# Kernel tuning notes

Measured on AMD Instinct MI355X. Metric: run time of the kernel, lower is better.

Reference implementation:

```python
import jax, jax.numpy as jnp
import numpy as np


def setup_inputs() -> dict:
    key = jax.random.key(0)
    k1, k2, k3 = jax.random.split(key, 3)
    x = jax.random.normal(k1, (16, 64, 256, 256), dtype=jnp.float32)
    # Conv2d(2, 1, kernel_size=7, padding=3): weight [out=1, in=2, 7, 7], bias [1]
    fan_in = 2 * 7 * 7
    bound = 1.0 / np.sqrt(fan_in)
    conv_w = jax.random.uniform(k2, (1, 2, 7, 7), jnp.float32, -bound, bound)
    conv_b = jax.random.uniform(k3, (1,), jnp.float32, -bound, bound)
    return {"x": x, "conv_w": conv_w, "conv_b": conv_b}


def reference(x, conv_w, conv_b):
    # x: [B, C, H, W]
    avg_out = jnp.mean(x, axis=1, keepdims=True)          # [B,1,H,W]
    max_out = jnp.max(x, axis=1, keepdims=True)           # [B,1,H,W]
    att = jnp.concatenate([avg_out, max_out], axis=1)     # [B,2,H,W]
    att = jax.lax.conv_general_dilated(
        att, conv_w,
        window_strides=(1, 1),
        padding=((3, 3), (3, 3)),
        dimension_numbers=("NCHW", "OIHW", "NCHW"),
    ) + conv_b.reshape(1, 1, 1, 1)                         # [B,1,H,W]
    att = jax.nn.sigmoid(att)
    return x * att
```

## Files before the change

kernel.cpp:

```cpp
#include <hip/hip_runtime.h>
#include <math.h>

#define BB   16
#define CC   64
#define HH_  256
#define WW_  256
#define HW   (HH_ * WW_)
#define CHW  (CC * HW)
#define BH   8
#define HALO 3
#define PR   (BH + 2*HALO)
#define NBANDS (HH_ / BH)
#define NBLK (BB * NBANDS)
#define NT_  512

typedef float vfloat4 __attribute__((ext_vector_type(4)));

__global__ __launch_bounds__(NT_) void fused_kernel(const float* __restrict__ x,
                                                    const float* __restrict__ cw,
                                                    const float* __restrict__ cb,
                                                    float* __restrict__ out) {
    __shared__ float sw[99];
    __shared__ float ap[PR][WW_];
    __shared__ float mp[PR][WW_];

    const int tid = threadIdx.x;
    if (tid < 99) sw[tid] = (tid < 98) ? cw[tid] : cb[0];

    const int bid  = blockIdx.x;
    const int b    = bid >> 5;
    const int band = bid & (NBANDS - 1);
    const int R0   = band * BH;

    const float4* xb4 = (const float4*)x + (size_t)b * (CHW / 4);

    for (int j = tid; j < PR * 64; j += NT_) {
        const int i   = j >> 6;
        const int q   = j & 63;
        const int row = R0 - HALO + i;
        float4 a = {0.f, 0.f, 0.f, 0.f};
        float4 m = {0.f, 0.f, 0.f, 0.f};
        if (row >= 0 && row < HH_) {
            const float4* p = xb4 + row * 64 + q;
            float4 s  = {0.f, 0.f, 0.f, 0.f};
            float4 mm = {-INFINITY, -INFINITY, -INFINITY, -INFINITY};
            #pragma unroll 8
            for (int c = 0; c < CC; ++c) {
                float4 v = p[c * (HW / 4)];
                s.x += v.x; s.y += v.y; s.z += v.z; s.w += v.w;
                mm.x = fmaxf(mm.x, v.x); mm.y = fmaxf(mm.y, v.y);
                mm.z = fmaxf(mm.z, v.z); mm.w = fmaxf(mm.w, v.w);
            }
            const float inv = 1.0f / 64.0f;
            a.x = s.x * inv; a.y = s.y * inv; a.z = s.z * inv; a.w = s.w * inv;
            m = mm;
        }
        *(float4*)&ap[i][q * 4] = a;
        *(float4*)&mp[i][q * 4] = m;
    }
    __syncthreads();

    const float bias = sw[98];

    {
        const int rl  = tid >> 6;
        const int q   = tid & 63;
        const int row = R0 + rl;

        float acc0 = bias, acc1 = bias, acc2 = bias, acc3 = bias;
        #pragma unroll
        for (int dy = -3; dy <= 3; ++dy) {
            const int li = rl + HALO + dy;
            const float4* a4 = (const float4*)&ap[li][0];
            const float4* m4 = (const float4*)&mp[li][0];
            const float4 z = {0.f, 0.f, 0.f, 0.f};
            float4 aL = (q > 0)  ? a4[q - 1] : z;
            float4 aC = a4[q];
            float4 aR = (q < 63) ? a4[q + 1] : z;
            float4 mL = (q > 0)  ? m4[q - 1] : z;
            float4 mC = m4[q];
            float4 mR = (q < 63) ? m4[q + 1] : z;
            float av[12] = {aL.x,aL.y,aL.z,aL.w, aC.x,aC.y,aC.z,aC.w, aR.x,aR.y,aR.z,aR.w};
            float mv[12] = {mL.x,mL.y,mL.z,mL.w, mC.x,mC.y,mC.z,mC.w, mR.x,mR.y,mR.z,mR.w};
            const float* wr = sw + (dy + 3) * 7;
            #pragma unroll
            for (int kx = 0; kx < 7; ++kx) {
                float wa = wr[kx];
                float wm = wr[49 + kx];
                int t = 1 + kx;
                acc0 = fmaf(av[t + 0], wa, acc0);  acc0 = fmaf(mv[t + 0], wm, acc0);
                acc1 = fmaf(av[t + 1], wa, acc1);  acc1 = fmaf(mv[t + 1], wm, acc1);
                acc2 = fmaf(av[t + 2], wa, acc2);  acc2 = fmaf(mv[t + 2], wm, acc2);
                acc3 = fmaf(av[t + 3], wa, acc3);  acc3 = fmaf(mv[t + 3], wm, acc3);
            }
        }

        const float att0 = 1.f / (1.f + __expf(-acc0));
        const float att1 = 1.f / (1.f + __expf(-acc1));
        const float att2 = 1.f / (1.f + __expf(-acc2));
        const float att3 = 1.f / (1.f + __expf(-acc3));

        const vfloat4* xr = (const vfloat4*)x  + (size_t)b * (CHW / 4) + row * 64 + q;
        vfloat4*       ow = (vfloat4*)out      + (size_t)b * (CHW / 4) + row * 64 + q;
        #pragma unroll 4
        for (int c = 0; c < CC; ++c) {
            vfloat4 v = __builtin_nontemporal_load(xr + c * (HW / 4));
            vfloat4 r;
            r.x = v.x * att0; r.y = v.y * att1; r.z = v.z * att2; r.w = v.w * att3;
            __builtin_nontemporal_store(r, ow + c * (HW / 4));
        }
    }
}

extern "C" void kernel_launch(void* const* d_in, const int* in_sizes, int n_in,
                              void* d_out, int out_size, void* d_ws, size_t ws_size,
                              hipStream_t stream) {
    const float* x  = (const float*)d_in[0];
    const float* cw = (const float*)d_in[1];
    const float* cb = (const float*)d_in[2];
    float* out = (float*)d_out;

    fused_kernel<<<dim3(NBLK), dim3(NT_), 0, stream>>>(x, cw, cb, out);
}
```

Measured before the change: 499.8 us.

## Split fused kernel into pool-conv kernel and grid-stride reverse-order scale kernel

Splits the single fused kernel into two. The first computes channel pooling, the 7x7 conv and the sigmoid, using smaller bands (4 rows, 256 threads, twice as many blocks), and writes the attention map to workspace. The second is a flat elementwise scale kernel that walks the tensor in reverse order, so the most recently read part of x is more likely to still be in cache. This raises parallelism in both phases but adds a kernel launch, a round trip of the attention map through memory, and more halo recomputation from the smaller bands.

```diff
diff --git a/kernel.cpp b/kernel.cpp
--- a/kernel.cpp
+++ b/kernel.cpp
@@ -7,19 +7,26 @@
 #define WW_  256
 #define HW   (HH_ * WW_)
 #define CHW  (CC * HW)
-#define BH   8
+#define NPIX (BB * HW)
+
+#define BH   4
 #define HALO 3
 #define PR   (BH + 2*HALO)
 #define NBANDS (HH_ / BH)
 #define NBLK (BB * NBANDS)
-#define NT_  512
+
+#define T4      (NPIX * CC / 4)
+#define K2_BLK  2048
+#define K2_THR  256
+#define K2_STEP (K2_BLK * K2_THR)
+#define K2_IT   (T4 / K2_STEP)
 
 typedef float vfloat4 __attribute__((ext_vector_type(4)));
 
-__global__ __launch_bounds__(NT_) void fused_kernel(const float* __restrict__ x,
-                                                    const float* __restrict__ cw,
-                                                    const float* __restrict__ cb,
-                                                    float* __restrict__ out) {
+__global__ __launch_bounds__(256) void pool_conv_kernel(const float* __restrict__ x,
+                                                        const float* __restrict__ cw,
+                                                        const float* __restrict__ cb,
+                                                        float* __restrict__ att) {
     __shared__ float sw[99];
     __shared__ float ap[PR][WW_];
     __shared__ float mp[PR][WW_];
@@ -28,13 +35,13 @@
     if (tid < 99) sw[tid] = (tid < 98) ? cw[tid] : cb[0];
 
     const int bid  = blockIdx.x;
-    const int b    = bid >> 5;
+    const int b    = bid >> 6;
     const int band = bid & (NBANDS - 1);
     const int R0   = band * BH;
 
     const float4* xb4 = (const float4*)x + (size_t)b * (CHW / 4);
 
-    for (int j = tid; j < PR * 64; j += NT_) {
+    for (int j = tid; j < PR * 64; j += 256) {
         const int i   = j >> 6;
         const int q   = j & 63;
         const int row = R0 - HALO + i;
@@ -44,7 +51,7 @@
             const float4* p = xb4 + row * 64 + q;
             float4 s  = {0.f, 0.f, 0.f, 0.f};
             float4 mm = {-INFINITY, -INFINITY, -INFINITY, -INFINITY};
-            #pragma unroll 8
+            #pragma unroll 16
             for (int c = 0; c < CC; ++c) {
                 float4 v = p[c * (HW / 4)];
                 s.x += v.x; s.y += v.y; s.z += v.z; s.w += v.w;
@@ -61,54 +68,64 @@
     __syncthreads();
 
     const float bias = sw[98];
+    const int rl  = tid >> 6;
+    const int q   = tid & 63;
+    const int row = R0 + rl;
 
-    {
-        const int rl  = tid >> 6;
-        const int q   = tid & 63;
-        const int row = R0 + rl;
+    float acc0 = bias, acc1 = bias, acc2 = bias, acc3 = bias;
+    #pragma unroll
+    for (int dy = -3; dy <= 3; ++dy) {
+        const int li = rl + HALO + dy;
+        const float4* a4 = (const float4*)&ap[li][0];
+        const float4* m4 = (const float4*)&mp[li][0];
+        const float4 z = {0.f, 0.f, 0.f, 0.f};
+        float4 aL = (q > 0)  ? a4[q - 1] : z;
+        float4 aC = a4[q];
+        float4 aR = (q < 63) ? a4[q + 1] : z;
+        float4 mL = (q > 0)  ? m4[q - 1] : z;
+        float4 mC = m4[q];
+        float4 mR = (q < 63) ? m4[q + 1] : z;
+        float av[12] = {aL.x,aL.y,aL.z,aL.w, aC.x,aC.y,aC.z,aC.w, aR.x,aR.y,aR.z,aR.w};
+        float mv[12] = {mL.x,mL.y,mL.z,mL.w, mC.x,mC.y,mC.z,mC.w, mR.x,mR.y,mR.z,mR.w};
+        const float* wr = sw + (dy + 3) * 7;
+        #pragma unroll
+        for (int kx = 0; kx < 7; ++kx) {
+            float wa = wr[kx];
+            float wm = wr[49 + kx];
+            int t = 1 + kx;
+            acc0 = fmaf(av[t + 0], wa, acc0);  acc0 = fmaf(mv[t + 0], wm, acc0);
+            acc1 = fmaf(av[t + 1], wa, acc1);  acc1 = fmaf(mv[t + 1], wm, acc1);
+            acc2 = fmaf(av[t + 2], wa, acc2);  acc2 = fmaf(mv[t + 2], wm, acc2);
+            acc3 = fmaf(av[t + 3], wa, acc3);  acc3 = fmaf(mv[t + 3], wm, acc3);
+        }
+    }
 
-        float acc0 = bias, acc1 = bias, acc2 = bias, acc3 = bias;
-        #pragma unroll
-        for (int dy = -3; dy <= 3; ++dy) {
-            const int li = rl + HALO + dy;
-            const float4* a4 = (const float4*)&ap[li][0];
-            const float4* m4 = (const float4*)&mp[li][0];
-            const float4 z = {0.f, 0.f, 0.f, 0.f};
-            float4 aL = (q > 0)  ? a4[q - 1] : z;
-            float4 aC = a4[q];
-            float4 aR = (q < 63) ? a4[q + 1] : z;
-            float4 mL = (q > 0)  ? m4[q - 1] : z;
-            float4 mC = m4[q];
-            float4 mR = (q < 63) ? m4[q + 1] : z;
-            float av[12] = {aL.x,aL.y,aL.z,aL.w, aC.x,aC.y,aC.z,aC.w, aR.x,aR.y,aR.z,aR.w};
-            float mv[12] = {mL.x,mL.y,mL.z,mL.w, mC.x,mC.y,mC.z,mC.w, mR.x,mR.y,mR.z,mR.w};
-            const float* wr = sw + (dy + 3) * 7;
-            #pragma unroll
-            for (int kx = 0; kx < 7; ++kx) {
-                float wa = wr[kx];
-                float wm = wr[49 + kx];
-                int t = 1 + kx;
-                acc0 = fmaf(av[t + 0], wa, acc0);  acc0 = fmaf(mv[t + 0], wm, acc0);
-                acc1 = fmaf(av[t + 1], wa, acc1);  acc1 = fmaf(mv[t + 1], wm, acc1);
-                acc2 = fmaf(av[t + 2], wa, acc2);  acc2 = fmaf(mv[t + 2], wm, acc2);
-                acc3 = fmaf(av[t + 3], wa, acc3);  acc3 = fmaf(mv[t + 3], wm, acc3);
-            }
-        }
+    float4 attq;
+    attq.x = 1.f / (1.f + __expf(-acc0));
+    attq.y = 1.f / (1.f + __expf(-acc1));
+    attq.z = 1.f / (1.f + __expf(-acc2));
+    attq.w = 1.f / (1.f + __expf(-acc3));
+    ((float4*)att)[b * (HW / 4) + row * 64 + q] = attq;
+}
 
-        const float att0 = 1.f / (1.f + __expf(-acc0));
-        const float att1 = 1.f / (1.f + __expf(-acc1));
-        const float att2 = 1.f / (1.f + __expf(-acc2));
-        const float att3 = 1.f / (1.f + __expf(-acc3));
+__global__ __launch_bounds__(K2_THR) void scale_kernel(const float* __restrict__ x,
+                                                       const float* __restrict__ att,
+                                                       float* __restrict__ out) {
+    const int rbid = gridDim.x - 1 - blockIdx.x;
+    const int lane = rbid * K2_THR + threadIdx.x;
+    const vfloat4* x4   = (const vfloat4*)x;
+    const vfloat4* att4 = (const vfloat4*)att;
+    vfloat4*       o4   = (vfloat4*)out;
 
-        const vfloat4* xr = (const vfloat4*)x  + (size_t)b * (CHW / 4) + row * 64 + q;
-        vfloat4*       ow = (vfloat4*)out      + (size_t)b * (CHW / 4) + row * 64 + q;
-        #pragma unroll 4
-        for (int c = 0; c < CC; ++c) {
-            vfloat4 v = __builtin_nontemporal_load(xr + c * (HW / 4));
-            vfloat4 r;
-            r.x = v.x * att0; r.y = v.y * att1; r.z = v.z * att2; r.w = v.w * att3;
-            __builtin_nontemporal_store(r, ow + c * (HW / 4));
-        }
+    for (int s = K2_IT - 1; s >= 0; --s) {
+        const int j  = s * K2_STEP + lane;
+        const int b  = j >> 20;
+        const int p4 = j & 16383;
+        vfloat4 v = __builtin_nontemporal_load(x4 + j);
+        vfloat4 a = att4[b * (HW / 4) + p4];
+        vfloat4 r;
+        r.x = v.x * a.x; r.y = v.y * a.y; r.z = v.z * a.z; r.w = v.w * a.w;
+        __builtin_nontemporal_store(r, o4 + j);
     }
 }
 
@@ -120,5 +137,8 @@
     const float* cb = (const float*)d_in[2];
     float* out = (float*)d_out;
 
-    fused_kernel<<<dim3(NBLK), dim3(NT_), 0, stream>>>(x, cw, cb, out);
+    float* att = (float*)d_ws;
+
+    pool_conv_kernel<<<dim3(NBLK), dim3(256), 0, stream>>>(x, cw, cb, att);
+    scale_kernel<<<dim3(K2_BLK), dim3(K2_THR), 0, stream>>>(x, att, out);
 }
```

Result: slower. 528.4 us (+5.7%).
